# Performance work log

Measured on AMD Instinct MI355X. Metric: run time of the kernel, lower is better.

The kernel has to match this reference:

```python
import jax, jax.numpy as jnp
import numpy as np

D_MODEL = 1024
N_HEADS = 16
D_K = D_MODEL // N_HEADS
SEQ = 4096
BATCH = 2
THETA = 10000.0


def _rope(x, token_positions):
    # x: [b, h, s, d_k], token_positions: [s] int
    half = D_K // 2
    inv_freq = 1.0 / (THETA ** (jnp.arange(0, D_K, 2, dtype=jnp.float32) / D_K))  # [half]
    freqs = token_positions.astype(jnp.float32)[:, None] * inv_freq[None, :]      # [s, half]
    cos, sin = jnp.cos(freqs), jnp.sin(freqs)                                     # [s, half]
    xe = x[..., 0::2]
    xo = x[..., 1::2]
    out_e = xe * cos - xo * sin
    out_o = xe * sin + xo * cos
    # interleave even/odd back: [..., s, half, 2] -> [..., s, d_k]
    return jnp.stack([out_e, out_o], axis=-1).reshape(x.shape)


def setup_inputs() -> dict:
    key = jax.random.key(0)
    ks = jax.random.split(key, 5)
    std = (2.0 / (D_MODEL + D_MODEL)) ** 0.5
    x = jax.random.normal(ks[0], (BATCH, SEQ, D_MODEL), dtype=jnp.float32)
    Wq = jax.random.normal(ks[1], (D_MODEL, D_MODEL), dtype=jnp.float32) * std
    Wk = jax.random.normal(ks[2], (D_MODEL, D_MODEL), dtype=jnp.float32) * std
    Wv = jax.random.normal(ks[3], (D_MODEL, D_MODEL), dtype=jnp.float32) * std
    Wo = jax.random.normal(ks[4], (D_MODEL, D_MODEL), dtype=jnp.float32) * std
    token_positions = jnp.arange(SEQ, dtype=jnp.int32)
    return {"x": x, "token_positions": token_positions, "Wq": Wq, "Wk": Wk, "Wv": Wv, "Wo": Wo}


def reference(x, token_positions, Wq, Wk, Wv, Wo):
    B, S, _ = x.shape

    def proj(W):
        y = jnp.einsum('bsd,od->bso', x, W)                     # [b, s, d_model]
        return y.reshape(B, S, N_HEADS, D_K).transpose(0, 2, 1, 3)  # [b, h, s, d_k]

    q, k, v = proj(Wq), proj(Wk), proj(Wv)
    q = _rope(q, token_positions)
    k = _rope(k, token_positions)

    scale = 1.0 / np.sqrt(D_K).astype(np.float32)
    scores = jnp.einsum('bhqd,bhkd->bhqk', q, k) * scale        # [b, h, s, s]
    causal = jnp.tril(jnp.ones((S, S), dtype=bool))
    scores = jnp.where(causal[None, None], scores, -jnp.inf)
    probs = jax.nn.softmax(scores, axis=-1)
    out = jnp.einsum('bhqk,bhkd->bhqd', probs, v)               # [b, h, s, d_k]
    out = out.transpose(0, 2, 1, 3).reshape(B, S, D_MODEL)
    return jnp.einsum('bsd,od->bso', out, Wo)
```

## Files before the change

kernel.cpp:

```cpp
#include <hip/hip_runtime.h>
#include <hip/hip_bf16.h>

typedef unsigned short u16;
typedef __attribute__((ext_vector_type(4))) float f32x4;
typedef __attribute__((ext_vector_type(16))) float f32x16;
typedef __attribute__((ext_vector_type(8))) short s16x8;
typedef __attribute__((ext_vector_type(2))) unsigned u32x2;

constexpr int DMODEL = 1024;
constexpr int NH     = 16;
constexpr int DK     = 64;
constexpr int SEQ    = 4096;
constexpr int BATCH  = 2;
constexpr int BS     = BATCH * SEQ;
constexpr int NX     = BS * DMODEL;
constexpr int NW     = DMODEL * DMODEL;
constexpr float QSC  = 0.18033688011112042f;

__device__ __forceinline__ unsigned pk2(float a, float b) {
  float2 t; t.x = a; t.y = b;
  __hip_bfloat162 h = __float22bfloat162_rn(t);
  return *reinterpret_cast<unsigned*>(&h);
}
__device__ __forceinline__ u32x2 plswap(unsigned a, unsigned b) {
  return __builtin_amdgcn_permlane32_swap(a, b, false, false);
}
__device__ __forceinline__ f32x16 mfma32(s16x8 a, s16x8 b, f32x16 c) {
  return __builtin_amdgcn_mfma_f32_32x32x16_bf16(a, b, c, 0, 0, 0);
}
__device__ __forceinline__ void gload_lds16(const void* g, void* l) {
  __builtin_amdgcn_global_load_lds(
      (const __attribute__((address_space(1))) void*)g,
      (__attribute__((address_space(3))) void*)l, 16, 0, 0);
}
__device__ __forceinline__ float exp2raw(float x) {
  return __builtin_amdgcn_exp2f(x);
}

constexpr int NTCONV = (NX + 4 * NW) / 4 / 256;
__global__ __launch_bounds__(256) void convert_all(
    const float* __restrict__ x, const float* __restrict__ wq,
    const float* __restrict__ wk, const float* __restrict__ wv,
    const float* __restrict__ wo, u16* __restrict__ xb, u16* __restrict__ Wb,
    const int* __restrict__ pos, float2* __restrict__ tab) {
  if (blockIdx.x >= NTCONV) {
    int t = (blockIdx.x - NTCONV) * 256 + threadIdx.x;
    const int s = t >> 5, i = t & 31;
    const float inv = expf(-(float)i * 0.28782313662425574f);
    const float ang = (float)pos[s] * inv;
    float sn, cs;
    sincosf(ang, &sn, &cs);
    tab[t] = make_float2(cs, sn);
    return;
  }
  int t = blockIdx.x * 256 + threadIdx.x;
  int i = t * 4;
  const float* src; u16* dst;
  if (i < NX) { src = x + i; dst = xb + i; }
  else {
    int j = i - NX; int w = j >> 20; int jj = j & (NW - 1);
    src = (w == 0 ? wq : w == 1 ? wk : w == 2 ? wv : wo) + jj;
    dst = Wb + j;
  }
  float4 v = *reinterpret_cast<const float4*>(src);
  uint2 pk; pk.x = pk2(v.x, v.y); pk.y = pk2(v.z, v.w);
  *reinterpret_cast<uint2*>(dst) = pk;
}

template <int EPI>
__global__ __launch_bounds__(256) void gemm128(
    const u16* __restrict__ A, const u16* __restrict__ B,
    u16* __restrict__ Qw, u16* __restrict__ Kw, u16* __restrict__ Vt,
    float* __restrict__ Co, const float2* __restrict__ tab) {
  __shared__ u16 lA[128 * 32];
  __shared__ u16 lB[128 * 32];
  const int tid = threadIdx.x, w = tid >> 6, l = tid & 63;
  const int wr = w >> 1, wc = w & 1;
  const int m0 = blockIdx.y * 128, n0 = blockIdx.x * 128;
  constexpr int K = 1024;
  f32x4 acc[4][4] = {};
  const int li = l & 15, lg = l >> 4;
  const int srow = l >> 2, skc = (l & 3) * 8;
  for (int k0 = 0; k0 < K; k0 += 32) {
    __syncthreads();
#pragma unroll
    for (int cc = 0; cc < 2; ++cc) {
      const int c = 2 * w + cc;
      const int row = c * 16 + srow;
      gload_lds16(A + (size_t)(m0 + row) * K + k0 + skc, &lA[c * 512]);
      gload_lds16(B + (size_t)(n0 + row) * K + k0 + skc, &lB[c * 512]);
    }
    __syncthreads();
    s16x8 af[4], bfr[4];
#pragma unroll
    for (int i = 0; i < 4; ++i)
      af[i] = *reinterpret_cast<const s16x8*>(&lA[(wr * 64 + i * 16 + li) * 32 + lg * 8]);
#pragma unroll
    for (int j = 0; j < 4; ++j)
      bfr[j] = *reinterpret_cast<const s16x8*>(&lB[(wc * 64 + j * 16 + li) * 32 + lg * 8]);
#pragma unroll
    for (int i = 0; i < 4; ++i)
#pragma unroll
      for (int j = 0; j < 4; ++j) {
        if (EPI == 1)
          acc[i][j] = __builtin_amdgcn_mfma_f32_16x16x32_bf16(af[i], bfr[j], acc[i][j], 0, 0, 0);
        else
          acc[i][j] = __builtin_amdgcn_mfma_f32_16x16x32_bf16(bfr[j], af[i], acc[i][j], 0, 0, 0);
      }
  }
#pragma unroll
  for (int i = 0; i < 4; ++i) {
#pragma unroll
    for (int j = 0; j < 4; ++j) {
      if (EPI == 0) {
        const int m = m0 + wr * 64 + i * 16 + li;
        const int bb = m >> 12, s = m & (SEQ - 1);
        const int n = n0 + wc * 64 + j * 16 + lg * 4;
        const int which = n >> 10, nn = n & 1023, h = nn >> 6, d0 = nn & 63;
        const int i0 = d0 >> 1;
        const float2 cs0 = tab[s * 32 + i0];
        const float2 cs1 = tab[s * 32 + i0 + 1];
        float oe0 = acc[i][j][0] * cs0.x - acc[i][j][1] * cs0.y;
        float oo0 = acc[i][j][0] * cs0.y + acc[i][j][1] * cs0.x;
        float oe1 = acc[i][j][2] * cs1.x - acc[i][j][3] * cs1.y;
        float oo1 = acc[i][j][2] * cs1.y + acc[i][j][3] * cs1.x;
        if (which == 0) { oe0 *= QSC; oo0 *= QSC; oe1 *= QSC; oo1 *= QSC; }
        u16* dst = (which == 0 ? Qw : Kw) + ((size_t)(bb * NH + h) * SEQ + s) * DK + d0;
        uint2 pk; pk.x = pk2(oe0, oo0); pk.y = pk2(oe1, oo1);
        *reinterpret_cast<uint2*>(dst) = pk;
      } else if (EPI == 1) {
        const int mbase = m0 + wr * 64 + i * 16 + lg * 4;
        const int b = mbase >> 12, s0 = mbase & (SEQ - 1);
        const int n = n0 + wc * 64 + j * 16 + li;
        const int h = n >> 6, d = n & 63;
        u16* dst = Vt + ((size_t)(b * NH + h) * DK + d) * SEQ + s0;
        uint2 pk;
        pk.x = pk2(acc[i][j][0], acc[i][j][1]);
        pk.y = pk2(acc[i][j][2], acc[i][j][3]);
        *reinterpret_cast<uint2*>(dst) = pk;
      } else {
        const int m = m0 + wr * 64 + i * 16 + li;
        const int n = n0 + wc * 64 + j * 16 + lg * 4;
        float4 v;
        v.x = acc[i][j][0]; v.y = acc[i][j][1]; v.z = acc[i][j][2]; v.w = acc[i][j][3];
        *reinterpret_cast<float4*>(&Co[(size_t)m * DMODEL + n]) = v;
      }
    }
  }
}

__global__ __launch_bounds__(256, 2) void attn_kernel(
    const u16* __restrict__ Qw, const u16* __restrict__ Kw,
    const u16* __restrict__ Vt, u16* __restrict__ Ob) {
  __shared__ __align__(16) u16 Kb[2][8192];
  __shared__ __align__(16) u16 Vb[2][8192];
  const int tid = threadIdx.x, w = tid >> 6, l = tid & 63;
  const int lq = l & 31, hi = l >> 5;
  const int id = blockIdx.x;
  const int g = (id & 7) * 64 + (id >> 3);
  const int bh = g >> 4;
  const int j  = g & 15;
  const int tA = 31 - j, tB = j;
  const int nA = 32 - j;
  const int ntot = 33;
  const u16* Qh = Qw + (size_t)bh * SEQ * DK;
  const u16* Kh = Kw + (size_t)bh * SEQ * DK;
  const u16* Vh = Vt + (size_t)bh * DK * SEQ;
  const int b = bh >> 4, h = bh & 15;

  const s16x8 ones = {(short)0x3F80, (short)0x3F80, (short)0x3F80, (short)0x3F80,
                      (short)0x3F80, (short)0x3F80, (short)0x3F80, (short)0x3F80};

  s16x8 aq[4];
  f32x16 o0, o1, ls;

  auto loadQ = [&](int q0) {
#pragma unroll
    for (int ds = 0; ds < 4; ++ds)
      aq[ds] = *reinterpret_cast<const s16x8*>(
          &Qh[(size_t)(q0 + lq) * DK + ds * 16 + hi * 8]);
  };
  auto resetState = [&]() { o0 = f32x16{}; o1 = f32x16{}; ls = f32x16{}; };
  auto writeO = [&](int q0) {
    const float inv = 1.f / ls[0];
    u16* orow = Ob + ((size_t)(b * SEQ + q0 + lq)) * DMODEL + h * DK;
#pragma unroll
    for (int m = 0; m < 4; ++m) {
      uint2 pa;
      pa.x = pk2(o0[4 * m + 0] * inv, o0[4 * m + 1] * inv);
      pa.y = pk2(o0[4 * m + 2] * inv, o0[4 * m + 3] * inv);
      *reinterpret_cast<uint2*>(orow + 8 * m + 4 * hi) = pa;
      uint2 pb;
      pb.x = pk2(o1[4 * m + 0] * inv, o1[4 * m + 1] * inv);
      pb.y = pk2(o1[4 * m + 2] * inv, o1[4 * m + 3] * inv);
      *reinterpret_cast<uint2*>(orow + 32 + 8 * m + 4 * hi) = pb;
    }
  };
  auto stageK = [&](int buf, int kt) {
    const int krow = tid >> 3;
    const int kcol = ((tid & 7) * 16) ^ ((krow & 7) << 4);
#pragma unroll
    for (int i = 0; i < 4; ++i)
      gload_lds16((const char*)Kh + (size_t)(kt + i * 32 + krow) * 128 + kcol,
                  (char*)&Kb[buf][0] + i * 4096 + tid * 16);
  };
  auto stageV = [&](int buf, int kt) {
    const int vrow = tid >> 4;
    const int vcol = ((tid & 15) * 16) ^ ((vrow & 7) << 4);
#pragma unroll
    for (int i = 0; i < 4; ++i)
      gload_lds16((const char*)Vh + (size_t)(i * 16 + vrow) * (SEQ * 2) + kt * 2 + vcol,
                  (char*)&Vb[buf][0] + i * 4096 + tid * 16);
  };

  int q0 = tA * 128 + w * 32;
  loadQ(q0);
  resetState();
  stageK(0, 0);
  stageV(0, 0);
  int kt = 0;
  for (int it = 0; it < ntot; ++it) {
    asm volatile("s_waitcnt vmcnt(4)" ::: "memory");
    __builtin_amdgcn_s_barrier();
    __builtin_amdgcn_sched_barrier(0);
    const int itn = it + 1;
    const int ktn = (itn < nA) ? 128 * itn : (itn < ntot ? 128 * (itn - nA) : 0);
    stageK(itn & 1, ktn);
    const int cur = it & 1;
    s16x8 p[2][4];
    const bool live0 = (kt <= q0 + 31);
    const bool live1 = (kt + 64 <= q0 + 31);
#pragma unroll
    for (int sub = 0; sub < 2; ++sub) {
      if (!(sub == 0 ? live0 : live1)) continue;
      const int ksub = kt + sub * 64;
      f32x16 s0 = {}, s1 = {};
      const char* kb = (const char*)&Kb[cur][0] + (sub * 64 + lq) * 128;
      __builtin_amdgcn_s_setprio(1);
#pragma unroll
      for (int ds = 0; ds < 4; ++ds) {
        const int co = (ds * 32 + hi * 16) ^ ((lq & 7) << 4);
        s16x8 k0 = *reinterpret_cast<const s16x8*>(kb + co);
        s16x8 k1 = *reinterpret_cast<const s16x8*>(kb + 32 * 128 + co);
        s0 = mfma32(k0, aq[ds], s0);
        s1 = mfma32(k1, aq[ds], s1);
      }
      __builtin_amdgcn_s_setprio(0);
      if (ksub + 63 > q0) {
#pragma unroll
        for (int r = 0; r < 16; ++r) {
          const int kr = (r & 3) + 8 * (r >> 2) + 4 * hi;
          if (ksub + kr > q0 + lq) s0[r] = -1e30f;
          if (ksub + 32 + kr > q0 + lq) s1[r] = -1e30f;
        }
      }
#pragma unroll
      for (int r = 0; r < 16; ++r) s0[r] = exp2raw(s0[r]);
#pragma unroll
      for (int r = 0; r < 16; ++r) s1[r] = exp2raw(s1[r]);
      unsigned U0[8], U1[8];
#pragma unroll
      for (int m = 0; m < 4; ++m) {
        U0[m * 2 + 0] = pk2(s0[4 * m + 0], s0[4 * m + 1]);
        U0[m * 2 + 1] = pk2(s0[4 * m + 2], s0[4 * m + 3]);
        U1[m * 2 + 0] = pk2(s1[4 * m + 0], s1[4 * m + 1]);
        U1[m * 2 + 1] = pk2(s1[4 * m + 2], s1[4 * m + 3]);
      }
#pragma unroll
      for (int c16 = 0; c16 < 4; ++c16) {
        unsigned* U = (c16 < 2) ? U0 : U1;
        const int m0i = (c16 & 1) * 2, m1i = m0i + 1;
        u32x2 r0 = plswap(U[m0i * 2 + 0], U[m1i * 2 + 0]);
        u32x2 r1 = plswap(U[m0i * 2 + 1], U[m1i * 2 + 1]);
        union { uint4 u; s16x8 s; } cf;
        cf.u.x = r0.x; cf.u.y = r1.x; cf.u.z = r0.y; cf.u.w = r1.y;
        p[sub][c16] = cf.s;
      }
    }
    asm volatile("s_waitcnt vmcnt(4)" ::: "memory");
    __builtin_amdgcn_s_barrier();
    __builtin_amdgcn_sched_barrier(0);
    stageV(itn & 1, ktn);
    const char* vb = (const char*)&Vb[cur][0];
#pragma unroll
    for (int sub = 0; sub < 2; ++sub) {
      if (!(sub == 0 ? live0 : live1)) continue;
      __builtin_amdgcn_s_setprio(1);
#pragma unroll
      for (int c16 = 0; c16 < 4; ++c16) {
        const int co = (sub * 128 + c16 * 32 + hi * 16) ^ ((lq & 7) << 4);
        s16x8 v0 = *reinterpret_cast<const s16x8*>(vb + lq * 256 + co);
        s16x8 v1 = *reinterpret_cast<const s16x8*>(vb + (32 + lq) * 256 + co);
        o0 = mfma32(v0, p[sub][c16], o0);
        o1 = mfma32(v1, p[sub][c16], o1);
        ls = mfma32(ones, p[sub][c16], ls);
      }
      __builtin_amdgcn_s_setprio(0);
    }
    if (it == nA - 1) {
      writeO(q0);
      q0 = tB * 128 + w * 32;
      loadQ(q0);
      resetState();
    }
    kt = ktn;
  }
  writeO(q0);
}

extern "C" void kernel_launch(void* const* d_in, const int* in_sizes, int n_in,
                              void* d_out, int out_size, void* d_ws, size_t ws_size,
                              hipStream_t stream) {
  const float* x  = (const float*)d_in[0];
  const int*  pos = (const int*)d_in[1];
  const float* wq = (const float*)d_in[2];
  const float* wk = (const float*)d_in[3];
  const float* wv = (const float*)d_in[4];
  const float* wo = (const float*)d_in[5];
  float* out = (float*)d_out;

  u16* Wb = (u16*)d_ws;
  u16* xb = Wb + 4 * (size_t)NW;
  u16* Qw = xb + (size_t)NX;
  u16* Kw = Qw + (size_t)NX;
  u16* Vt = Kw + (size_t)NX;
  float2* tab = (float2*)(Vt + (size_t)NX);
  u16* Ab = xb;

  convert_all<<<NTCONV + 512, 256, 0, stream>>>(x, wq, wk, wv, wo, xb, Wb, pos, tab);
  gemm128<0><<<dim3(16, 64), 256, 0, stream>>>(xb, Wb, Qw, Kw, nullptr, nullptr, tab);
  gemm128<1><<<dim3(8, 64), 256, 0, stream>>>(xb, Wb + 2 * (size_t)NW, nullptr, nullptr, Vt, nullptr, nullptr);
  attn_kernel<<<512, 256, 0, stream>>>(Qw, Kw, Vt, Ab);
  gemm128<2><<<dim3(8, 64), 256, 0, stream>>>(Ab, Wb + 3 * (size_t)NW, nullptr, nullptr, nullptr, out, nullptr);
}
```

Baseline: 236.0 us.

## Split attention key tile across warp pairs with 64-row query blocks and LDS reduction

Reorganizes the attention kernel so each warp handles 64 query rows and one 64-key half of the 128-key tile, instead of 32 query rows over all keys. K and V fragments are loaded once into registers and reused across two query sub-blocks. Partial outputs and row sums from the two key-half warps are combined through shared memory at flush time. K and V staging is merged into one stage per iteration with a single full vmcnt(0) wait and barrier, which reduces synchronization but may expose more load latency and raises register pressure.

```diff
diff --git a/kernel.cpp b/kernel.cpp
--- a/kernel.cpp
+++ b/kernel.cpp
@@ -154,8 +154,10 @@
     const u16* __restrict__ Vt, u16* __restrict__ Ob) {
   __shared__ __align__(16) u16 Kb[2][8192];
   __shared__ __align__(16) u16 Vb[2][8192];
+  __shared__ float lsred[2][2][64];
   const int tid = threadIdx.x, w = tid >> 6, l = tid & 63;
   const int lq = l & 31, hi = l >> 5;
+  const int wq = w >> 1, wk = w & 1;
   const int id = blockIdx.x;
   const int g = (id & 7) * 64 + (id >> 3);
   const int bh = g >> 4;
@@ -171,40 +173,29 @@
   const s16x8 ones = {(short)0x3F80, (short)0x3F80, (short)0x3F80, (short)0x3F80,
                       (short)0x3F80, (short)0x3F80, (short)0x3F80, (short)0x3F80};
 
-  s16x8 aq[4];
-  f32x16 o0, o1, ls;
+  s16x8 aq[2][4];
+  f32x16 o[2][2];
+  f32x16 ls[2];
 
   auto loadQ = [&](int q0) {
 #pragma unroll
-    for (int ds = 0; ds < 4; ++ds)
-      aq[ds] = *reinterpret_cast<const s16x8*>(
-          &Qh[(size_t)(q0 + lq) * DK + ds * 16 + hi * 8]);
+    for (int qh = 0; qh < 2; ++qh)
+#pragma unroll
+      for (int ds = 0; ds < 4; ++ds)
+        aq[qh][ds] = *reinterpret_cast<const s16x8*>(
+            &Qh[(size_t)(q0 + wq * 64 + qh * 32 + lq) * DK + ds * 16 + hi * 8]);
   };
-  auto resetState = [&]() { o0 = f32x16{}; o1 = f32x16{}; ls = f32x16{}; };
-  auto writeO = [&](int q0) {
-    const float inv = 1.f / ls[0];
-    u16* orow = Ob + ((size_t)(b * SEQ + q0 + lq)) * DMODEL + h * DK;
-#pragma unroll
-    for (int m = 0; m < 4; ++m) {
-      uint2 pa;
-      pa.x = pk2(o0[4 * m + 0] * inv, o0[4 * m + 1] * inv);
-      pa.y = pk2(o0[4 * m + 2] * inv, o0[4 * m + 3] * inv);
-      *reinterpret_cast<uint2*>(orow + 8 * m + 4 * hi) = pa;
-      uint2 pb;
-      pb.x = pk2(o1[4 * m + 0] * inv, o1[4 * m + 1] * inv);
-      pb.y = pk2(o1[4 * m + 2] * inv, o1[4 * m + 3] * inv);
-      *reinterpret_cast<uint2*>(orow + 32 + 8 * m + 4 * hi) = pb;
-    }
+  auto resetState = [&]() {
+    o[0][0] = f32x16{}; o[0][1] = f32x16{}; o[1][0] = f32x16{}; o[1][1] = f32x16{};
+    ls[0] = f32x16{}; ls[1] = f32x16{};
   };
-  auto stageK = [&](int buf, int kt) {
+  auto stage = [&](int buf, int kt) {
     const int krow = tid >> 3;
     const int kcol = ((tid & 7) * 16) ^ ((krow & 7) << 4);
 #pragma unroll
     for (int i = 0; i < 4; ++i)
       gload_lds16((const char*)Kh + (size_t)(kt + i * 32 + krow) * 128 + kcol,
                   (char*)&Kb[buf][0] + i * 4096 + tid * 16);
-  };
-  auto stageV = [&](int buf, int kt) {
     const int vrow = tid >> 4;
     const int vcol = ((tid & 15) * 16) ^ ((vrow & 7) << 4);
 #pragma unroll
@@ -212,100 +203,151 @@
       gload_lds16((const char*)Vh + (size_t)(i * 16 + vrow) * (SEQ * 2) + kt * 2 + vcol,
                   (char*)&Vb[buf][0] + i * 4096 + tid * 16);
   };
-
-  int q0 = tA * 128 + w * 32;
+  auto flush = [&](int q0f, int cb) {
+    __syncthreads();
+    float* os = (float*)(wq == 0 ? &Kb[cb][0] : &Vb[cb][0]);
+    if (wk == 1) {
+#pragma unroll
+      for (int dh = 0; dh < 2; ++dh)
+#pragma unroll
+        for (int qh = 0; qh < 2; ++qh)
+#pragma unroll
+          for (int r = 0; r < 16; ++r)
+            os[((dh * 2 + qh) * 16 + r) * 64 + l] = o[dh][qh][r];
+      lsred[wq][0][l] = ls[0][0];
+      lsred[wq][1][l] = ls[1][0];
+    }
+    __syncthreads();
+    if (wk == 0) {
+      float inv[2];
+#pragma unroll
+      for (int qh = 0; qh < 2; ++qh)
+        inv[qh] = 1.f / (ls[qh][0] + lsred[wq][qh][l]);
+#pragma unroll
+      for (int dh = 0; dh < 2; ++dh)
+#pragma unroll
+        for (int qh = 0; qh < 2; ++qh)
+#pragma unroll
+          for (int r = 0; r < 16; ++r)
+            o[dh][qh][r] += os[((dh * 2 + qh) * 16 + r) * 64 + l];
+#pragma unroll
+      for (int qh = 0; qh < 2; ++qh) {
+        u16* orow = Ob + ((size_t)(b * SEQ + q0f + wq * 64 + qh * 32 + lq)) * DMODEL + h * DK;
+#pragma unroll
+        for (int dh = 0; dh < 2; ++dh)
+#pragma unroll
+          for (int m = 0; m < 4; ++m) {
+            uint2 pa;
+            pa.x = pk2(o[dh][qh][4 * m + 0] * inv[qh], o[dh][qh][4 * m + 1] * inv[qh]);
+            pa.y = pk2(o[dh][qh][4 * m + 2] * inv[qh], o[dh][qh][4 * m + 3] * inv[qh]);
+            *reinterpret_cast<uint2*>(orow + dh * 32 + 8 * m + 4 * hi) = pa;
+          }
+      }
+    }
+  };
+
+  int q0 = tA * 128;
   loadQ(q0);
   resetState();
-  stageK(0, 0);
-  stageV(0, 0);
+  stage(0, 0);
   int kt = 0;
   for (int it = 0; it < ntot; ++it) {
-    asm volatile("s_waitcnt vmcnt(4)" ::: "memory");
+    asm volatile("s_waitcnt vmcnt(0)" ::: "memory");
     __builtin_amdgcn_s_barrier();
     __builtin_amdgcn_sched_barrier(0);
     const int itn = it + 1;
     const int ktn = (itn < nA) ? 128 * itn : (itn < ntot ? 128 * (itn - nA) : 0);
-    stageK(itn & 1, ktn);
+    stage(itn & 1, ktn);
     const int cur = it & 1;
-    s16x8 p[2][4];
-    const bool live0 = (kt <= q0 + 31);
-    const bool live1 = (kt + 64 <= q0 + 31);
-#pragma unroll
-    for (int sub = 0; sub < 2; ++sub) {
-      if (!(sub == 0 ? live0 : live1)) continue;
-      const int ksub = kt + sub * 64;
-      f32x16 s0 = {}, s1 = {};
-      const char* kb = (const char*)&Kb[cur][0] + (sub * 64 + lq) * 128;
+    const int qb0 = q0 + wq * 64;
+    const int kb0 = kt + wk * 64;
+    if (kb0 <= qb0 + 63) {
+      const int sw = (lq & 7) << 4;
+      s16x8 kf[2][4];
+      const char* kbase = (const char*)&Kb[cur][0] + (size_t)(wk * 64 + lq) * 128;
+#pragma unroll
+      for (int kh = 0; kh < 2; ++kh)
+#pragma unroll
+        for (int ds = 0; ds < 4; ++ds)
+          kf[kh][ds] = *reinterpret_cast<const s16x8*>(
+              kbase + kh * 32 * 128 + ((ds * 32 + hi * 16) ^ sw));
+      s16x8 p[2][4];
+      const bool diag = (kb0 + 63 > qb0);
+#pragma unroll
+      for (int qh = 0; qh < 2; ++qh) {
+        f32x16 s0 = {}, s1 = {};
+        __builtin_amdgcn_s_setprio(1);
+#pragma unroll
+        for (int ds = 0; ds < 4; ++ds) {
+          s0 = mfma32(kf[0][ds], aq[qh][ds], s0);
+          s1 = mfma32(kf[1][ds], aq[qh][ds], s1);
+        }
+        __builtin_amdgcn_s_setprio(0);
+        if (diag) {
+          const int qq = qb0 + qh * 32 + lq;
+#pragma unroll
+          for (int r = 0; r < 16; ++r) {
+            const int kr = (r & 3) + 8 * (r >> 2) + 4 * hi;
+            if (kb0 + kr > qq) s0[r] = -1e30f;
+            if (kb0 + 32 + kr > qq) s1[r] = -1e30f;
+          }
+        }
+#pragma unroll
+        for (int r = 0; r < 16; ++r) s0[r] = exp2raw(s0[r]);
+#pragma unroll
+        for (int r = 0; r < 16; ++r) s1[r] = exp2raw(s1[r]);
+        unsigned U0[8], U1[8];
+#pragma unroll
+        for (int m = 0; m < 4; ++m) {
+          U0[m * 2 + 0] = pk2(s0[4 * m + 0], s0[4 * m + 1]);
+          U0[m * 2 + 1] = pk2(s0[4 * m + 2], s0[4 * m + 3]);
+          U1[m * 2 + 0] = pk2(s1[4 * m + 0], s1[4 * m + 1]);
+          U1[m * 2 + 1] = pk2(s1[4 * m + 2], s1[4 * m + 3]);
+        }
+#pragma unroll
+        for (int c16 = 0; c16 < 4; ++c16) {
+          unsigned* U = (c16 < 2) ? U0 : U1;
+          const int m0i = (c16 & 1) * 2, m1i = m0i + 1;
+          u32x2 r0 = plswap(U[m0i * 2 + 0], U[m1i * 2 + 0]);
+          u32x2 r1 = plswap(U[m0i * 2 + 1], U[m1i * 2 + 1]);
+          union { uint4 u; s16x8 s; } cf;
+          cf.u.x = r0.x; cf.u.y = r1.x; cf.u.z = r0.y; cf.u.w = r1.y;
+          p[qh][c16] = cf.s;
+        }
+      }
+      const char* vb = (const char*)&Vb[cur][0];
+#pragma unroll
+      for (int dh = 0; dh < 2; ++dh) {
+        s16x8 vf[4];
+#pragma unroll
+        for (int c16 = 0; c16 < 4; ++c16)
+          vf[c16] = *reinterpret_cast<const s16x8*>(
+              vb + (size_t)(dh * 32 + lq) * 256 + ((wk * 128 + c16 * 32 + hi * 16) ^ sw));
+        __builtin_amdgcn_s_setprio(1);
+#pragma unroll
+        for (int qh = 0; qh < 2; ++qh)
+#pragma unroll
+          for (int c16 = 0; c16 < 4; ++c16)
+            o[dh][qh] = mfma32(vf[c16], p[qh][c16], o[dh][qh]);
+        __builtin_amdgcn_s_setprio(0);
+      }
       __builtin_amdgcn_s_setprio(1);
 #pragma unroll
-      for (int ds = 0; ds < 4; ++ds) {
-        const int co = (ds * 32 + hi * 16) ^ ((lq & 7) << 4);
-        s16x8 k0 = *reinterpret_cast<const s16x8*>(kb + co);
-        s16x8 k1 = *reinterpret_cast<const s16x8*>(kb + 32 * 128 + co);
-        s0 = mfma32(k0, aq[ds], s0);
-        s1 = mfma32(k1, aq[ds], s1);
-      }
+      for (int qh = 0; qh < 2; ++qh)
+#pragma unroll
+        for (int c16 = 0; c16 < 4; ++c16)
+          ls[qh] = mfma32(ones, p[qh][c16], ls[qh]);
       __builtin_amdgcn_s_setprio(0);
-      if (ksub + 63 > q0) {
-#pragma unroll
-        for (int r = 0; r < 16; ++r) {
-          const int kr = (r & 3) + 8 * (r >> 2) + 4 * hi;
-          if (ksub + kr > q0 + lq) s0[r] = -1e30f;
-          if (ksub + 32 + kr > q0 + lq) s1[r] = -1e30f;
-        }
-      }
-#pragma unroll
-      for (int r = 0; r < 16; ++r) s0[r] = exp2raw(s0[r]);
-#pragma unroll
-      for (int r = 0; r < 16; ++r) s1[r] = exp2raw(s1[r]);
-      unsigned U0[8], U1[8];
-#pragma unroll
-      for (int m = 0; m < 4; ++m) {
-        U0[m * 2 + 0] = pk2(s0[4 * m + 0], s0[4 * m + 1]);
-        U0[m * 2 + 1] = pk2(s0[4 * m + 2], s0[4 * m + 3]);
-        U1[m * 2 + 0] = pk2(s1[4 * m + 0], s1[4 * m + 1]);
-        U1[m * 2 + 1] = pk2(s1[4 * m + 2], s1[4 * m + 3]);
-      }
-#pragma unroll
-      for (int c16 = 0; c16 < 4; ++c16) {
-        unsigned* U = (c16 < 2) ? U0 : U1;
-        const int m0i = (c16 & 1) * 2, m1i = m0i + 1;
-        u32x2 r0 = plswap(U[m0i * 2 + 0], U[m1i * 2 + 0]);
-        u32x2 r1 = plswap(U[m0i * 2 + 1], U[m1i * 2 + 1]);
-        union { uint4 u; s16x8 s; } cf;
-        cf.u.x = r0.x; cf.u.y = r1.x; cf.u.z = r0.y; cf.u.w = r1.y;
-        p[sub][c16] = cf.s;
-      }
-    }
-    asm volatile("s_waitcnt vmcnt(4)" ::: "memory");
-    __builtin_amdgcn_s_barrier();
-    __builtin_amdgcn_sched_barrier(0);
-    stageV(itn & 1, ktn);
-    const char* vb = (const char*)&Vb[cur][0];
-#pragma unroll
-    for (int sub = 0; sub < 2; ++sub) {
-      if (!(sub == 0 ? live0 : live1)) continue;
-      __builtin_amdgcn_s_setprio(1);
-#pragma unroll
-      for (int c16 = 0; c16 < 4; ++c16) {
-        const int co = (sub * 128 + c16 * 32 + hi * 16) ^ ((lq & 7) << 4);
-        s16x8 v0 = *reinterpret_cast<const s16x8*>(vb + lq * 256 + co);
-        s16x8 v1 = *reinterpret_cast<const s16x8*>(vb + (32 + lq) * 256 + co);
-        o0 = mfma32(v0, p[sub][c16], o0);
-        o1 = mfma32(v1, p[sub][c16], o1);
-        ls = mfma32(ones, p[sub][c16], ls);
-      }
-      __builtin_amdgcn_s_setprio(0);
     }
     if (it == nA - 1) {
-      writeO(q0);
-      q0 = tB * 128 + w * 32;
+      flush(q0, cur);
+      q0 = tB * 128;
       loadQ(q0);
       resetState();
     }
     kt = ktn;
   }
-  writeO(q0);
+  flush(q0, (ntot - 1) & 1);
 }
 
 extern "C" void kernel_launch(void* const* d_in, const int* in_sizes, int n_in,
```

Measured after the change: 272.2 us. 1.15x slower.

## Merge QKV GEMM launches and fuse K/V staging into single barrier per tile

Applied to the files above, without the earlier changes.

Combines the separate QK and V projection GEMMs into one launch with a 24-column grid, where blocks pick their weight slice and epilogue by column index. This removes one kernel launch and the tail of the smaller launch. In the attention kernel, K and V tiles are now staged together behind a single wait-for-all-loads barrier instead of two partial-wait barriers. The PV MFMAs are interleaved directly after each softmax chunk instead of being held in a P register array. This cuts a barrier and some register pressure, but waiting on vmcnt(0) may expose more load latency because V prefetch is no longer overlapped with QK compute.

```diff
diff --git a/kernel.cpp b/kernel.cpp
--- a/kernel.cpp
+++ b/kernel.cpp
@@ -67,16 +67,18 @@
   *reinterpret_cast<uint2*>(dst) = pk;
 }
 
-template <int EPI>
-__global__ __launch_bounds__(256) void gemm128(
-    const u16* __restrict__ A, const u16* __restrict__ B,
+__global__ __launch_bounds__(256) void gemm_qkv(
+    const u16* __restrict__ A, const u16* __restrict__ Wb,
     u16* __restrict__ Qw, u16* __restrict__ Kw, u16* __restrict__ Vt,
-    float* __restrict__ Co, const float2* __restrict__ tab) {
+    const float2* __restrict__ tab) {
   __shared__ u16 lA[128 * 32];
   __shared__ u16 lB[128 * 32];
   const int tid = threadIdx.x, w = tid >> 6, l = tid & 63;
   const int wr = w >> 1, wc = w & 1;
-  const int m0 = blockIdx.y * 128, n0 = blockIdx.x * 128;
+  const bool isV = blockIdx.x >= 16;
+  const int m0 = blockIdx.y * 128;
+  const int n0 = (isV ? (int)blockIdx.x - 16 : (int)blockIdx.x) * 128;
+  const u16* B = Wb + (isV ? 2 * (size_t)NW : 0);
   constexpr int K = 1024;
   f32x4 acc[4][4] = {};
   const int li = l & 15, lg = l >> 4;
@@ -98,21 +100,25 @@
 #pragma unroll
     for (int j = 0; j < 4; ++j)
       bfr[j] = *reinterpret_cast<const s16x8*>(&lB[(wc * 64 + j * 16 + li) * 32 + lg * 8]);
-#pragma unroll
-    for (int i = 0; i < 4; ++i)
+    if (isV) {
+#pragma unroll
+      for (int i = 0; i < 4; ++i)
+#pragma unroll
+        for (int j = 0; j < 4; ++j)
+          acc[i][j] = __builtin_amdgcn_mfma_f32_16x16x32_bf16(af[i], bfr[j], acc[i][j], 0, 0, 0);
+    } else {
+#pragma unroll
+      for (int i = 0; i < 4; ++i)
+#pragma unroll
+        for (int j = 0; j < 4; ++j)
+          acc[i][j] = __builtin_amdgcn_mfma_f32_16x16x32_bf16(bfr[j], af[i], acc[i][j], 0, 0, 0);
+    }
+  }
+  if (!isV) {
+#pragma unroll
+    for (int i = 0; i < 4; ++i) {
 #pragma unroll
       for (int j = 0; j < 4; ++j) {
-        if (EPI == 1)
-          acc[i][j] = __builtin_amdgcn_mfma_f32_16x16x32_bf16(af[i], bfr[j], acc[i][j], 0, 0, 0);
-        else
-          acc[i][j] = __builtin_amdgcn_mfma_f32_16x16x32_bf16(bfr[j], af[i], acc[i][j], 0, 0, 0);
-      }
-  }
-#pragma unroll
-  for (int i = 0; i < 4; ++i) {
-#pragma unroll
-    for (int j = 0; j < 4; ++j) {
-      if (EPI == 0) {
         const int m = m0 + wr * 64 + i * 16 + li;
         const int bb = m >> 12, s = m & (SEQ - 1);
         const int n = n0 + wc * 64 + j * 16 + lg * 4;
@@ -128,7 +134,13 @@
         u16* dst = (which == 0 ? Qw : Kw) + ((size_t)(bb * NH + h) * SEQ + s) * DK + d0;
         uint2 pk; pk.x = pk2(oe0, oo0); pk.y = pk2(oe1, oo1);
         *reinterpret_cast<uint2*>(dst) = pk;
-      } else if (EPI == 1) {
+      }
+    }
+  } else {
+#pragma unroll
+    for (int i = 0; i < 4; ++i) {
+#pragma unroll
+      for (int j = 0; j < 4; ++j) {
         const int mbase = m0 + wr * 64 + i * 16 + lg * 4;
         const int b = mbase >> 12, s0 = mbase & (SEQ - 1);
         const int n = n0 + wc * 64 + j * 16 + li;
@@ -138,13 +150,54 @@
         pk.x = pk2(acc[i][j][0], acc[i][j][1]);
         pk.y = pk2(acc[i][j][2], acc[i][j][3]);
         *reinterpret_cast<uint2*>(dst) = pk;
-      } else {
-        const int m = m0 + wr * 64 + i * 16 + li;
-        const int n = n0 + wc * 64 + j * 16 + lg * 4;
-        float4 v;
-        v.x = acc[i][j][0]; v.y = acc[i][j][1]; v.z = acc[i][j][2]; v.w = acc[i][j][3];
-        *reinterpret_cast<float4*>(&Co[(size_t)m * DMODEL + n]) = v;
-      }
+      }
+    }
+  }
+}
+
+__global__ __launch_bounds__(256) void gemm_out(
+    const u16* __restrict__ A, const u16* __restrict__ B, float* __restrict__ Co) {
+  __shared__ u16 lA[128 * 32];
+  __shared__ u16 lB[128 * 32];
+  const int tid = threadIdx.x, w = tid >> 6, l = tid & 63;
+  const int wr = w >> 1, wc = w & 1;
+  const int m0 = blockIdx.y * 128, n0 = blockIdx.x * 128;
+  constexpr int K = 1024;
+  f32x4 acc[4][4] = {};
+  const int li = l & 15, lg = l >> 4;
+  const int srow = l >> 2, skc = (l & 3) * 8;
+  for (int k0 = 0; k0 < K; k0 += 32) {
+    __syncthreads();
+#pragma unroll
+    for (int cc = 0; cc < 2; ++cc) {
+      const int c = 2 * w + cc;
+      const int row = c * 16 + srow;
+      gload_lds16(A + (size_t)(m0 + row) * K + k0 + skc, &lA[c * 512]);
+      gload_lds16(B + (size_t)(n0 + row) * K + k0 + skc, &lB[c * 512]);
+    }
+    __syncthreads();
+    s16x8 af[4], bfr[4];
+#pragma unroll
+    for (int i = 0; i < 4; ++i)
+      af[i] = *reinterpret_cast<const s16x8*>(&lA[(wr * 64 + i * 16 + li) * 32 + lg * 8]);
+#pragma unroll
+    for (int j = 0; j < 4; ++j)
+      bfr[j] = *reinterpret_cast<const s16x8*>(&lB[(wc * 64 + j * 16 + li) * 32 + lg * 8]);
+#pragma unroll
+    for (int i = 0; i < 4; ++i)
+#pragma unroll
+      for (int j = 0; j < 4; ++j)
+        acc[i][j] = __builtin_amdgcn_mfma_f32_16x16x32_bf16(bfr[j], af[i], acc[i][j], 0, 0, 0);
+  }
+#pragma unroll
+  for (int i = 0; i < 4; ++i) {
+#pragma unroll
+    for (int j = 0; j < 4; ++j) {
+      const int m = m0 + wr * 64 + i * 16 + li;
+      const int n = n0 + wc * 64 + j * 16 + lg * 4;
+      float4 v;
+      v.x = acc[i][j][0]; v.y = acc[i][j][1]; v.z = acc[i][j][2]; v.w = acc[i][j][3];
+      *reinterpret_cast<float4*>(&Co[(size_t)m * DMODEL + n]) = v;
     }
   }
 }
@@ -196,15 +249,13 @@
       *reinterpret_cast<uint2*>(orow + 32 + 8 * m + 4 * hi) = pb;
     }
   };
-  auto stageK = [&](int buf, int kt) {
+  auto stage = [&](int buf, int kt) {
     const int krow = tid >> 3;
     const int kcol = ((tid & 7) * 16) ^ ((krow & 7) << 4);
 #pragma unroll
     for (int i = 0; i < 4; ++i)
       gload_lds16((const char*)Kh + (size_t)(kt + i * 32 + krow) * 128 + kcol,
                   (char*)&Kb[buf][0] + i * 4096 + tid * 16);
-  };
-  auto stageV = [&](int buf, int kt) {
     const int vrow = tid >> 4;
     const int vcol = ((tid & 15) * 16) ^ ((vrow & 7) << 4);
 #pragma unroll
@@ -216,24 +267,20 @@
   int q0 = tA * 128 + w * 32;
   loadQ(q0);
   resetState();
-  stageK(0, 0);
-  stageV(0, 0);
+  stage(0, 0);
   int kt = 0;
   for (int it = 0; it < ntot; ++it) {
-    asm volatile("s_waitcnt vmcnt(4)" ::: "memory");
+    asm volatile("s_waitcnt vmcnt(0)" ::: "memory");
     __builtin_amdgcn_s_barrier();
     __builtin_amdgcn_sched_barrier(0);
     const int itn = it + 1;
     const int ktn = (itn < nA) ? 128 * itn : (itn < ntot ? 128 * (itn - nA) : 0);
-    stageK(itn & 1, ktn);
+    stage(itn & 1, ktn);
     const int cur = it & 1;
-    s16x8 p[2][4];
-    const bool live0 = (kt <= q0 + 31);
-    const bool live1 = (kt + 64 <= q0 + 31);
 #pragma unroll
     for (int sub = 0; sub < 2; ++sub) {
-      if (!(sub == 0 ? live0 : live1)) continue;
       const int ksub = kt + sub * 64;
+      if (ksub > q0 + 31) continue;
       f32x16 s0 = {}, s1 = {};
       const char* kb = (const char*)&Kb[cur][0] + (sub * 64 + lq) * 128;
       __builtin_amdgcn_s_setprio(1);
@@ -266,6 +313,7 @@
         U1[m * 2 + 0] = pk2(s1[4 * m + 0], s1[4 * m + 1]);
         U1[m * 2 + 1] = pk2(s1[4 * m + 2], s1[4 * m + 3]);
       }
+      const char* vb = (const char*)&Vb[cur][0];
 #pragma unroll
       for (int c16 = 0; c16 < 4; ++c16) {
         unsigned* U = (c16 < 2) ? U0 : U1;
@@ -274,28 +322,15 @@
         u32x2 r1 = plswap(U[m0i * 2 + 1], U[m1i * 2 + 1]);
         union { uint4 u; s16x8 s; } cf;
         cf.u.x = r0.x; cf.u.y = r1.x; cf.u.z = r0.y; cf.u.w = r1.y;
-        p[sub][c16] = cf.s;
-      }
-    }
-    asm volatile("s_waitcnt vmcnt(4)" ::: "memory");
-    __builtin_amdgcn_s_barrier();
-    __builtin_amdgcn_sched_barrier(0);
-    stageV(itn & 1, ktn);
-    const char* vb = (const char*)&Vb[cur][0];
-#pragma unroll
-    for (int sub = 0; sub < 2; ++sub) {
-      if (!(sub == 0 ? live0 : live1)) continue;
-      __builtin_amdgcn_s_setprio(1);
-#pragma unroll
-      for (int c16 = 0; c16 < 4; ++c16) {
         const int co = (sub * 128 + c16 * 32 + hi * 16) ^ ((lq & 7) << 4);
         s16x8 v0 = *reinterpret_cast<const s16x8*>(vb + lq * 256 + co);
         s16x8 v1 = *reinterpret_cast<const s16x8*>(vb + (32 + lq) * 256 + co);
-        o0 = mfma32(v0, p[sub][c16], o0);
-        o1 = mfma32(v1, p[sub][c16], o1);
-        ls = mfma32(ones, p[sub][c16], ls);
-      }
-      __builtin_amdgcn_s_setprio(0);
+        __builtin_amdgcn_s_setprio(1);
+        o0 = mfma32(v0, cf.s, o0);
+        o1 = mfma32(v1, cf.s, o1);
+        ls = mfma32(ones, cf.s, ls);
+        __builtin_amdgcn_s_setprio(0);
+      }
     }
     if (it == nA - 1) {
       writeO(q0);
@@ -328,8 +363,7 @@
   u16* Ab = xb;
 
   convert_all<<<NTCONV + 512, 256, 0, stream>>>(x, wq, wk, wv, wo, xb, Wb, pos, tab);
-  gemm128<0><<<dim3(16, 64), 256, 0, stream>>>(xb, Wb, Qw, Kw, nullptr, nullptr, tab);
-  gemm128<1><<<dim3(8, 64), 256, 0, stream>>>(xb, Wb + 2 * (size_t)NW, nullptr, nullptr, Vt, nullptr, nullptr);
+  gemm_qkv<<<dim3(24, 64), 256, 0, stream>>>(xb, Wb, Qw, Kw, Vt, tab);
   attn_kernel<<<512, 256, 0, stream>>>(Qw, Kw, Vt, Ab);
-  gemm128<2><<<dim3(8, 64), 256, 0, stream>>>(Ab, Wb + 3 * (size_t)NW, nullptr, nullptr, nullptr, out, nullptr);
-}
+  gemm_out<<<dim3(8, 64), 256, 0, stream>>>(Ab, Wb + 3 * (size_t)NW, out);
+}
```

Result: faster. 229.8 us (-2.6%).
